# Kernel optimization log

Hardware: AMD Instinct MI355X
Metric: run time of the kernel (lower is better)

The kernel has to match this reference:

```python
import jax, jax.numpy as jnp
import numpy as np

N, E, IN_CH, HID, EDGE_DIM, L, G = 50000, 800000, 64, 128, 16, 3, 256

def _bn(h, g, b):
    # BatchNorm1d in training mode (biased batch variance), eps=1e-5
    m = h.mean(0)
    v = ((h - m) ** 2).mean(0)
    return (h - m) * jax.lax.rsqrt(v + 1e-5) * g + b

def setup_inputs() -> dict:
    key = jax.random.key(0)
    ks = jax.random.split(key, 24)
    s = 0.05
    inp = {
        'x': jax.random.normal(ks[0], (N, IN_CH), jnp.float32),
        'edge_attr': jax.random.uniform(ks[1], (E, EDGE_DIM), jnp.float32),
        'src': jax.random.randint(ks[2], (E,), 0, N, jnp.int32),
        'dst': jax.random.randint(ks[3], (E,), 0, N, jnp.int32),
        'batch': jnp.sort(jax.random.randint(ks[4], (N,), 0, G, jnp.int32)),
        'Wp': jax.random.normal(ks[5], (IN_CH, HID), jnp.float32) * s,
        'bp': jnp.zeros((HID,), jnp.float32),
        'conv_We': jax.random.normal(ks[6], (L, EDGE_DIM, HID), jnp.float32) * s,
        'conv_be': jnp.zeros((L, HID), jnp.float32),
        'conv_W1': jax.random.normal(ks[7], (L, HID, HID), jnp.float32) * s,
        'conv_b1': jnp.zeros((L, HID), jnp.float32),
        'conv_g1': jnp.ones((L, HID), jnp.float32),
        'conv_bt1': jnp.zeros((L, HID), jnp.float32),
        'conv_W2': jax.random.normal(ks[8], (L, HID, HID), jnp.float32) * s,
        'conv_b2': jnp.zeros((L, HID), jnp.float32),
        'bn_g': jnp.ones((L, HID), jnp.float32),
        'bn_b': jnp.zeros((L, HID), jnp.float32),
        'head_W1': jax.random.normal(ks[9], (HID * L * 2, HID), jnp.float32) * s,
        'head_b1': jnp.zeros((HID,), jnp.float32),
        'head_g': jnp.ones((HID,), jnp.float32),
        'head_bt': jnp.zeros((HID,), jnp.float32),
        'head_W2': jax.random.normal(ks[10], (HID, 1), jnp.float32) * s,
        'head_b2': jnp.zeros((1,), jnp.float32),
    }
    return inp

def reference(x, edge_attr, src, dst, batch, Wp, bp, conv_We, conv_be, conv_W1, conv_b1,
              conv_g1, conv_bt1, conv_W2, conv_b2, bn_g, bn_b, head_W1, head_b1,
              head_g, head_bt, head_W2, head_b2):
    n = x.shape[0]
    h = x @ Wp + bp  # [N, HID]
    outs = []
    for l in range(L):
        # GINEConv: msg = ReLU(x_src + lin(edge_attr)); sum-aggregate to dst; (1+eps)*x + agg, eps=0
        ee = edge_attr @ conv_We[l] + conv_be[l]          # [E, HID]
        msg = jax.nn.relu(h[src] + ee)                     # [E, HID]
        agg = jax.ops.segment_sum(msg, dst, num_segments=n)
        t = h + agg
        t = t @ conv_W1[l] + conv_b1[l]
        t = jax.nn.relu(_bn(t, conv_g1[l], conv_bt1[l]))
        t = t @ conv_W2[l] + conv_b2[l]
        h = jax.nn.relu(_bn(t, bn_g[l], bn_b[l]))          # outer BN + ReLU (dropout = identity, eval)
        outs.append(h)
    xj = jnp.concatenate(outs, axis=-1)                    # JK 'cat' -> [N, 3*HID]
    cnt = jax.ops.segment_sum(jnp.ones((n,), xj.dtype), batch, num_segments=G)
    z_mean = jax.ops.segment_sum(xj, batch, num_segments=G) / jnp.clip(cnt, 1.0)[:, None]
    z_max = jax.ops.segment_max(xj, batch, num_segments=G)
    z = jnp.concatenate([z_mean, z_max], axis=-1)          # [G, 6*HID]
    z = z @ head_W1 + head_b1
    z = jax.nn.relu(_bn(z, head_g, head_bt))
    return (z @ head_W2 + head_b2).squeeze(-1)             # [G]
```

## Files before the change

kernel.cpp:

```cpp
#include <hip/hip_runtime.h>
#include <hip/hip_bf16.h>
#include <hip/hip_fp16.h>

#define HID 128
#define EDIM 16

typedef float v4f __attribute__((ext_vector_type(4)));
typedef float v2f __attribute__((ext_vector_type(2)));
typedef short s8v __attribute__((ext_vector_type(8)));
typedef float f4v __attribute__((ext_vector_type(4)));
typedef unsigned int u8x __attribute__((ext_vector_type(8)));
typedef _Float16 h2v __attribute__((ext_vector_type(2)));

#define MFMA_BF16(a, b, c) __builtin_amdgcn_mfma_f32_16x16x32_bf16((a), (b), (c), 0, 0, 0)

__device__ __forceinline__ unsigned short bf16_rne(float v)
{
    unsigned u = __builtin_bit_cast(unsigned, v);
    return (unsigned short)((u + 0x7fffu + ((u >> 16) & 1u)) >> 16);
}

__device__ __forceinline__ unsigned pack2(float lo, float hi)
{
    return (unsigned)bf16_rne(lo) | ((unsigned)bf16_rne(hi) << 16);
}

__device__ __forceinline__ float bflo(unsigned u) { return __builtin_bit_cast(float, u << 16); }
__device__ __forceinline__ float bfhi(unsigned u) { return __builtin_bit_cast(float, u & 0xffff0000u); }

__device__ __forceinline__ v2f unpack2(unsigned u)
{
    v2f r; r.x = bflo(u); r.y = bfhi(u); return r;
}

__device__ __forceinline__ void split_bf16(float v, unsigned short& h, unsigned short& l)
{
    unsigned u = __builtin_bit_cast(unsigned, v);
    unsigned hu = (u + 0x7fffu + ((u >> 16) & 1u)) >> 16;
    h = (unsigned short)hu;
    float hf = __builtin_bit_cast(float, hu << 16);
    l = bf16_rne(v - hf);
}

__device__ __forceinline__ v2f vmax0(v2f a)
{
    v2f r; r.x = fmaxf(a.x, 0.f); r.y = fmaxf(a.y, 0.f); return r;
}

__device__ __forceinline__ unsigned pkh2(float lo, float hi)
{
    return (unsigned)__half_as_ushort(__float2half(lo)) |
           ((unsigned)__half_as_ushort(__float2half(hi)) << 16);
}

__device__ __forceinline__ void dot2(float& d, unsigned ea, unsigned w)
{
    d = __builtin_amdgcn_fdot2(__builtin_bit_cast(h2v, ea),
                               __builtin_bit_cast(h2v, w), d, false);
}

__global__ void hist_kernel(const int* __restrict__ dst, int* __restrict__ deg, int E)
{
    int e = blockIdx.x * 256 + threadIdx.x;
    if (e < E) atomicAdd(&deg[dst[e]], 1);
}

__global__ void block_sum_kernel(const int* __restrict__ deg, int* __restrict__ bsum, int Nn)
{
    int i = blockIdx.x * 256 + threadIdx.x;
    int v = (i < Nn) ? deg[i] : 0;
#pragma unroll
    for (int off = 32; off > 0; off >>= 1) v += __shfl_down(v, off, 64);
    __shared__ int ws[4];
    if ((threadIdx.x & 63) == 0) ws[threadIdx.x >> 6] = v;
    __syncthreads();
    if (threadIdx.x == 0) bsum[blockIdx.x] = ws[0] + ws[1] + ws[2] + ws[3];
}

__global__ void bsum_scan_kernel(int* bsum, int nb, int* total_out)
{
    __shared__ int sh[256];
    int tid = threadIdx.x;
    int v = (tid < nb) ? bsum[tid] : 0;
    sh[tid] = v;
    __syncthreads();
    for (int off = 1; off < 256; off <<= 1) {
        int tv = (tid >= off) ? sh[tid - off] : 0;
        __syncthreads();
        sh[tid] += tv;
        __syncthreads();
    }
    if (tid < nb) bsum[tid] = sh[tid] - v;
    if (tid == 255) *total_out = sh[255];
}

__global__ void block_scan_kernel(const int* __restrict__ deg, const int* __restrict__ bsum,
                                  int* __restrict__ row_start, int* __restrict__ cursor, int Nn)
{
    __shared__ int sh[256];
    int tid = threadIdx.x;
    int i = blockIdx.x * 256 + tid;
    int v = (i < Nn) ? deg[i] : 0;
    sh[tid] = v;
    __syncthreads();
    for (int off = 1; off < 256; off <<= 1) {
        int tv = (tid >= off) ? sh[tid - off] : 0;
        __syncthreads();
        sh[tid] += tv;
        __syncthreads();
    }
    if (i < Nn) {
        int excl = sh[tid] - v + bsum[blockIdx.x];
        row_start[i] = excl;
        cursor[i] = excl;
    }
}

__global__ void scatter_kernel(const int* __restrict__ src, const int* __restrict__ dst,
                               int* cursor, int* __restrict__ perm,
                               int* __restrict__ src_perm, int E)
{
    int e = blockIdx.x * 256 + threadIdx.x;
    if (e >= E) return;
    int pos = atomicAdd(&cursor[dst[e]], 1);
    perm[pos] = e;
    src_perm[pos] = src[e];
}

__global__ void gather_ea_f16(const float* __restrict__ ea, const int* __restrict__ perm,
                              unsigned* __restrict__ eaH, int E)
{
    int idx = blockIdx.x * 256 + threadIdx.x;
    int p = idx >> 1, hf = idx & 1;
    if (p >= E) return;
    int e = perm[p];
    const float* ap = &ea[(size_t)e * EDIM + hf * 8];
    float4 f0 = *(const float4*)ap;
    float4 f1 = *(const float4*)(ap + 4);
    uint4 o;
    o.x = pkh2(f0.x, f0.y);
    o.y = pkh2(f0.z, f0.w);
    o.z = pkh2(f1.x, f1.y);
    o.w = pkh2(f1.z, f1.w);
    *(uint4*)&eaH[(size_t)p * 8 + hf * 4] = o;
}

__global__ void prep_weights(const float* __restrict__ Wp, const float* __restrict__ W1,
                             const float* __restrict__ W2, unsigned short* __restrict__ out)
{
    int idx = blockIdx.x * 256 + threadIdx.x;
    if (idx < 8192) {
        int n = idx >> 6, k = idx & 63;
        unsigned short h, l;
        split_bf16(Wp[k * 128 + n], h, l);
        out[idx] = h;
        out[8192 + idx] = l;
    } else {
        int j = idx - 8192;
        if (j >= 6 * 16384) return;
        int m2 = j >> 14;
        int r = j & 16383;
        int n = r >> 7, k = r & 127;
        int l = m2 >> 1;
        const float* Wsrc = (m2 & 1) ? (W2 + l * 16384) : (W1 + l * 16384);
        unsigned short h, lo;
        split_bf16(Wsrc[k * 128 + n], h, lo);
        int base = 16384 + m2 * 32768;
        out[base + r] = h;
        out[base + 16384 + r] = lo;
    }
}

__device__ __forceinline__ void edge_f16(v2f& acc, v2f bj, unsigned hu, const u8x& e,
                                         const unsigned* __restrict__ wpk0,
                                         const unsigned* __restrict__ wpk1)
{
    float m0 = bj.x + bflo(hu);
    float m1 = bj.y + bfhi(hu);
#pragma unroll
    for (int kp = 0; kp < 8; ++kp) {
        dot2(m0, e[kp], wpk0[kp]);
        dot2(m1, e[kp], wpk1[kp]);
    }
    acc.x += fmaxf(m0, 0.f);
    acc.y += fmaxf(m1, 0.f);
}

__global__ __launch_bounds__(256, 8) void aggregate_f16(
    const unsigned short* __restrict__ h16, const unsigned* __restrict__ eaH,
    const int* __restrict__ src_perm, const int* __restrict__ row_start,
    const float* __restrict__ We, const float* __restrict__ be,
    float* __restrict__ t, int Nn)
{
    int tid = threadIdx.x;
    int lane = tid & 63;
    int c = lane * 2;
    unsigned wpk0[8], wpk1[8];
#pragma unroll
    for (int kp = 0; kp < 8; ++kp) {
        wpk0[kp] = pkh2(We[(2 * kp) * HID + c],     We[(2 * kp + 1) * HID + c]);
        wpk1[kp] = pkh2(We[(2 * kp) * HID + c + 1], We[(2 * kp + 1) * HID + c + 1]);
    }
    v2f bj = *(const v2f*)&be[c];
    int node = blockIdx.x * 4 + (tid >> 6);
    if (node >= Nn) return;
    const unsigned* __restrict__ hw = (const unsigned*)h16 + lane;
    v2f acc = unpack2(hw[(unsigned)node << 6]);
    int p0 = __builtin_amdgcn_readfirstlane(row_start[node]);
    int p1 = __builtin_amdgcn_readfirstlane(row_start[node + 1]);
    int p = p0;

    int s0 = 0, s1 = 0, s2 = 0, s3 = 0, s4 = 0, s5 = 0, s6 = 0, s7 = 0;
    unsigned hu0 = 0, hu1 = 0, hu2 = 0, hu3 = 0, hu4 = 0, hu5 = 0, hu6 = 0, hu7 = 0;
    if (p + 8 <= p1) {
        s0 = src_perm[p];     s1 = src_perm[p + 1]; s2 = src_perm[p + 2]; s3 = src_perm[p + 3];
        s4 = src_perm[p + 4]; s5 = src_perm[p + 5]; s6 = src_perm[p + 6]; s7 = src_perm[p + 7];
        hu0 = hw[(unsigned)s0 << 6]; hu1 = hw[(unsigned)s1 << 6];
        hu2 = hw[(unsigned)s2 << 6]; hu3 = hw[(unsigned)s3 << 6];
        hu4 = hw[(unsigned)s4 << 6]; hu5 = hw[(unsigned)s5 << 6];
        hu6 = hw[(unsigned)s6 << 6]; hu7 = hw[(unsigned)s7 << 6];
    }
    while (p + 8 <= p1) {
        int np = p + 8;
        u8x e0 = *(const u8x*)(eaH + (size_t)(unsigned)(p    ) * 8);
        u8x e1 = *(const u8x*)(eaH + (size_t)(unsigned)(p + 1) * 8);
        u8x e2 = *(const u8x*)(eaH + (size_t)(unsigned)(p + 2) * 8);
        u8x e3 = *(const u8x*)(eaH + (size_t)(unsigned)(p + 3) * 8);
        u8x e4 = *(const u8x*)(eaH + (size_t)(unsigned)(p + 4) * 8);
        u8x e5 = *(const u8x*)(eaH + (size_t)(unsigned)(p + 5) * 8);
        u8x e6 = *(const u8x*)(eaH + (size_t)(unsigned)(p + 6) * 8);
        u8x e7 = *(const u8x*)(eaH + (size_t)(unsigned)(p + 7) * 8);
        int t0 = 0, t1 = 0, t2 = 0, t3 = 0, t4 = 0, t5 = 0, t6 = 0, t7 = 0;
        unsigned hn0 = 0, hn1 = 0, hn2 = 0, hn3 = 0, hn4 = 0, hn5 = 0, hn6 = 0, hn7 = 0;
        if (np + 8 <= p1) {
            t0 = src_perm[np];     t1 = src_perm[np + 1]; t2 = src_perm[np + 2]; t3 = src_perm[np + 3];
            t4 = src_perm[np + 4]; t5 = src_perm[np + 5]; t6 = src_perm[np + 6]; t7 = src_perm[np + 7];
            hn0 = hw[(unsigned)t0 << 6]; hn1 = hw[(unsigned)t1 << 6];
            hn2 = hw[(unsigned)t2 << 6]; hn3 = hw[(unsigned)t3 << 6];
            hn4 = hw[(unsigned)t4 << 6]; hn5 = hw[(unsigned)t5 << 6];
            hn6 = hw[(unsigned)t6 << 6]; hn7 = hw[(unsigned)t7 << 6];
        }
        edge_f16(acc, bj, hu0, e0, wpk0, wpk1);
        edge_f16(acc, bj, hu1, e1, wpk0, wpk1);
        edge_f16(acc, bj, hu2, e2, wpk0, wpk1);
        edge_f16(acc, bj, hu3, e3, wpk0, wpk1);
        edge_f16(acc, bj, hu4, e4, wpk0, wpk1);
        edge_f16(acc, bj, hu5, e5, wpk0, wpk1);
        edge_f16(acc, bj, hu6, e6, wpk0, wpk1);
        edge_f16(acc, bj, hu7, e7, wpk0, wpk1);
        p = np;
        s0 = t0; s1 = t1; s2 = t2; s3 = t3; s4 = t4; s5 = t5; s6 = t6; s7 = t7;
        hu0 = hn0; hu1 = hn1; hu2 = hn2; hu3 = hn3;
        hu4 = hn4; hu5 = hn5; hu6 = hn6; hu7 = hn7;
    }
    for (; p < p1; ++p) {
        int s = src_perm[p];
        unsigned hu = hw[(unsigned)s << 6];
        u8x e = *(const u8x*)(eaH + (size_t)(unsigned)p * 8);
        edge_f16(acc, bj, hu, e, wpk0, wpk1);
    }
    *(v2f*)(t + ((unsigned)node << 7) + c) = acc;
}

__device__ __forceinline__ void matvp(const v4f& a0, const v4f& a1,
                                      const v4f& a2, const v4f& a3,
                                      const v2f* __restrict__ w, v2f& m)
{
    m += w[0] * a0.x;  m += w[1] * a0.y;  m += w[2] * a0.z;  m += w[3] * a0.w;
    m += w[4] * a1.x;  m += w[5] * a1.y;  m += w[6] * a1.z;  m += w[7] * a1.w;
    m += w[8] * a2.x;  m += w[9] * a2.y;  m += w[10] * a2.z; m += w[11] * a2.w;
    m += w[12] * a3.x; m += w[13] * a3.y; m += w[14] * a3.z; m += w[15] * a3.w;
}

__global__ __launch_bounds__(256, 8) void aggregate_fp32(
    const unsigned short* __restrict__ h16, const float* __restrict__ eaG,
    const int* __restrict__ perm, const int* __restrict__ src_perm,
    const int* __restrict__ row_start,
    const float* __restrict__ We, const float* __restrict__ be,
    float* __restrict__ t, int Nn)
{
    int tid = threadIdx.x;
    int lane = tid & 63;
    int c = lane * 2;
    v2f w[16];
#pragma unroll
    for (int k = 0; k < 16; ++k) w[k] = *(const v2f*)&We[k * HID + c];
    v2f bj = *(const v2f*)&be[c];
    int node = blockIdx.x * 4 + (tid >> 6);
    if (node >= Nn) return;
    const unsigned* __restrict__ hw = (const unsigned*)h16 + lane;
    v2f acc = unpack2(hw[(unsigned)node << 6]);
    int p0 = __builtin_amdgcn_readfirstlane(row_start[node]);
    int p1 = __builtin_amdgcn_readfirstlane(row_start[node + 1]);
    int p = p0;
    int s0 = 0, s1 = 0, s2 = 0, s3 = 0;
    if (p + 4 <= p1) { s0 = src_perm[p]; s1 = src_perm[p + 1]; s2 = src_perm[p + 2]; s3 = src_perm[p + 3]; }
    while (p + 4 <= p1) {
        int np = p + 4;
        int t0 = 0, t1 = 0, t2 = 0, t3 = 0;
        if (np + 4 <= p1) { t0 = src_perm[np]; t1 = src_perm[np + 1]; t2 = src_perm[np + 2]; t3 = src_perm[np + 3]; }
        unsigned hu0 = hw[(unsigned)s0 << 6];
        unsigned hu1 = hw[(unsigned)s1 << 6];
        unsigned hu2 = hw[(unsigned)s2 << 6];
        unsigned hu3 = hw[(unsigned)s3 << 6];
        int q0 = perm[p], q1 = perm[p + 1], q2 = perm[p + 2], q3 = perm[p + 3];
        const v4f* e0 = (const v4f*)(eaG + (size_t)(unsigned)q0 * EDIM);
        const v4f* e1 = (const v4f*)(eaG + (size_t)(unsigned)q1 * EDIM);
        const v4f* e2 = (const v4f*)(eaG + (size_t)(unsigned)q2 * EDIM);
        const v4f* e3 = (const v4f*)(eaG + (size_t)(unsigned)q3 * EDIM);
        v4f a00 = e0[0], a01 = e0[1], a02 = e0[2], a03 = e0[3];
        v4f a10 = e1[0], a11 = e1[1], a12 = e1[2], a13 = e1[3];
        v4f a20 = e2[0], a21 = e2[1], a22 = e2[2], a23 = e2[3];
        v4f a30 = e3[0], a31 = e3[1], a32 = e3[2], a33 = e3[3];
        v2f m0 = bj + unpack2(hu0), m1 = bj + unpack2(hu1);
        v2f m2 = bj + unpack2(hu2), m3 = bj + unpack2(hu3);
        matvp(a00, a01, a02, a03, w, m0);
        matvp(a10, a11, a12, a13, w, m1);
        matvp(a20, a21, a22, a23, w, m2);
        matvp(a30, a31, a32, a33, w, m3);
        acc += (vmax0(m0) + vmax0(m1)) + (vmax0(m2) + vmax0(m3));
        p = np;
        s0 = t0; s1 = t1; s2 = t2; s3 = t3;
    }
    for (; p < p1; ++p) {
        int s = src_perm[p];
        int q = perm[p];
        const v4f* e0 = (const v4f*)(eaG + (size_t)(unsigned)q * EDIM);
        v4f a0 = e0[0], a1 = e0[1], a2 = e0[2], a3 = e0[3];
        v2f m0 = bj + unpack2(hw[(unsigned)s << 6]);
        matvp(a0, a1, a2, a3, w, m0);
        acc += vmax0(m0);
    }
    *(v2f*)(t + ((unsigned)node << 7) + c) = acc;
}

#define LPAD 40

template<int K, bool PRE_BN, bool POST_STATS, bool OUT_BF16>
__global__ __launch_bounds__(256) void gemm_mfma(
    const float* __restrict__ A, const unsigned short* __restrict__ Wh,
    const unsigned short* __restrict__ Wl, const float* __restrict__ bias,
    const float* __restrict__ preStats, const float* __restrict__ preG, const float* __restrict__ preB,
    void* __restrict__ Cout, float* __restrict__ postStats, int Nrows, float invN)
{
    __shared__ __align__(16) unsigned short Ah[128 * LPAD], Al[128 * LPAD];
    __shared__ __align__(16) unsigned short Bh[128 * LPAD], Bl[128 * LPAD];
    __shared__ float sc[PRE_BN ? K : 1], sb[PRE_BN ? K : 1];
    int tid = threadIdx.x;
    int rbase = blockIdx.x * 128;
    if (PRE_BN) {
        if (tid < K) {
            float mean = preStats[tid] * invN;
            float var = preStats[K + tid] * invN - mean * mean;
            float rstd = rsqrtf(var + 1e-5f);
            float g = preG[tid];
            sc[tid] = rstd * g;
            sb[tid] = preB[tid] - mean * rstd * g;
        }
        __syncthreads();
    }
    int w = tid >> 6, nl = tid & 15, q = (tid >> 4) & 3;
    f4v acc[2][8];
#pragma unroll
    for (int mt = 0; mt < 2; ++mt)
#pragma unroll
        for (int nt = 0; nt < 8; ++nt)
#pragma unroll
            for (int r = 0; r < 4; ++r) acc[mt][nt][r] = 0.f;

    for (int ks = 0; ks < K / 32; ++ks) {
        int k0 = ks * 32;
        if (ks) __syncthreads();
#pragma unroll
        for (int i = 0; i < 4; ++i) {
            int cidx = tid + i * 256;
            int m = cidx >> 3, k4 = (cidx & 7) * 4;
            int gr = rbase + m;
            float4 v = make_float4(0.f, 0.f, 0.f, 0.f);
            if (gr < Nrows) v = *(const float4*)&A[(size_t)gr * K + k0 + k4];
            if (PRE_BN) {
                v.x = fmaxf(v.x * sc[k0 + k4]     + sb[k0 + k4],     0.f);
                v.y = fmaxf(v.y * sc[k0 + k4 + 1] + sb[k0 + k4 + 1], 0.f);
                v.z = fmaxf(v.z * sc[k0 + k4 + 2] + sb[k0 + k4 + 2], 0.f);
                v.w = fmaxf(v.w * sc[k0 + k4 + 3] + sb[k0 + k4 + 3], 0.f);
            }
            unsigned short h0, l0, h1, l1, h2, l2, h3, l3;
            split_bf16(v.x, h0, l0); split_bf16(v.y, h1, l1);
            split_bf16(v.z, h2, l2); split_bf16(v.w, h3, l3);
            uint2 hp, lp;
            hp.x = (unsigned)h0 | ((unsigned)h1 << 16); hp.y = (unsigned)h2 | ((unsigned)h3 << 16);
            lp.x = (unsigned)l0 | ((unsigned)l1 << 16); lp.y = (unsigned)l2 | ((unsigned)l3 << 16);
            *(uint2*)&Ah[m * LPAD + k4] = hp;
            *(uint2*)&Al[m * LPAD + k4] = lp;
        }
#pragma unroll
        for (int i = 0; i < 2; ++i) {
            int g = tid + i * 256;
            int n = g >> 2, kq = (g & 3) * 8;
            uint4 hv = *(const uint4*)&Wh[(size_t)n * K + k0 + kq];
            uint4 lv = *(const uint4*)&Wl[(size_t)n * K + k0 + kq];
            *(uint4*)&Bh[n * LPAD + kq] = hv;
            *(uint4*)&Bl[n * LPAD + kq] = lv;
        }
        __syncthreads();
        s8v ah0 = *(const s8v*)&Ah[(w * 32 + nl) * LPAD + q * 8];
        s8v ah1 = *(const s8v*)&Ah[(w * 32 + 16 + nl) * LPAD + q * 8];
        s8v al0 = *(const s8v*)&Al[(w * 32 + nl) * LPAD + q * 8];
        s8v al1 = *(const s8v*)&Al[(w * 32 + 16 + nl) * LPAD + q * 8];
#pragma unroll
        for (int nt = 0; nt < 8; ++nt) {
            s8v bh = *(const s8v*)&Bh[(nt * 16 + nl) * LPAD + q * 8];
            s8v bl = *(const s8v*)&Bl[(nt * 16 + nl) * LPAD + q * 8];
            acc[0][nt] = MFMA_BF16(ah0, bh, acc[0][nt]);
            acc[0][nt] = MFMA_BF16(ah0, bl, acc[0][nt]);
            acc[0][nt] = MFMA_BF16(al0, bh, acc[0][nt]);
            acc[1][nt] = MFMA_BF16(ah1, bh, acc[1][nt]);
            acc[1][nt] = MFMA_BF16(ah1, bl, acc[1][nt]);
            acc[1][nt] = MFMA_BF16(al1, bh, acc[1][nt]);
        }
    }
    __syncthreads();

    float* Cf = (float*)Cout;
    unsigned short* Ch = (unsigned short*)Cout;
    float* redS = (float*)Ah;
    float* redQ = (float*)Al;
#pragma unroll
    for (int nt = 0; nt < 8; ++nt) {
        int col = nt * 16 + nl;
        float bcol = bias[col];
        float sv = 0.f, qv = 0.f;
#pragma unroll
        for (int mt = 0; mt < 2; ++mt) {
#pragma unroll
            for (int r = 0; r < 4; ++r) {
                int grow = rbase + w * 32 + mt * 16 + q * 4 + r;
                if (grow < Nrows) {
                    float o = acc[mt][nt][r] + bcol;
                    if (OUT_BF16) Ch[(size_t)grow * HID + col] = bf16_rne(o);
                    else          Cf[(size_t)grow * HID + col] = o;
                    if (POST_STATS) { sv += o; qv += o * o; }
                }
            }
        }
        if (POST_STATS) {
            sv += __shfl_down(sv, 32, 64); sv += __shfl_down(sv, 16, 64);
            qv += __shfl_down(qv, 32, 64); qv += __shfl_down(qv, 16, 64);
            if ((tid & 63) < 16) { redS[w * 128 + col] = sv; redQ[w * 128 + col] = qv; }
        }
    }
    if (POST_STATS) {
        __syncthreads();
        if (tid < 128) {
            float S = redS[tid] + redS[128 + tid] + redS[256 + tid] + redS[384 + tid];
            float Q = redQ[tid] + redQ[128 + tid] + redQ[256 + tid] + redQ[384 + tid];
            atomicAdd(&postStats[tid], S);
            atomicAdd(&postStats[128 + tid], Q);
        }
    }
}

__global__ void bn_apply_pool(const float* __restrict__ X, unsigned short* __restrict__ h16,
                              const float* __restrict__ stats, const float* __restrict__ g,
                              const float* __restrict__ b, const int* __restrict__ starts,
                              float* __restrict__ z, int l, float invN)
{
    int gph = blockIdx.x;
    int tid = threadIdx.x;
    int ch4 = (tid & 31) * 4, wk = tid >> 5;
    float sc[4], sh[4];
#pragma unroll
    for (int u = 0; u < 4; ++u) {
        int j = ch4 + u;
        float mean = stats[j] * invN;
        float var = stats[128 + j] * invN - mean * mean;
        float rstd = rsqrtf(var + 1e-5f);
        float gg = g[j];
        sc[u] = rstd * gg;
        sh[u] = b[j] - mean * rstd * gg;
    }
    int s = starts[gph], e = starts[gph + 1];
    float4 sum = make_float4(0.f, 0.f, 0.f, 0.f);
    float4 mx = make_float4(0.f, 0.f, 0.f, 0.f);
    unsigned* hv32 = (unsigned*)h16;
    for (int n = s + wk; n < e; n += 16) {
        float4 v = *(const float4*)&X[(size_t)n * HID + ch4];
        v.x = fmaxf(v.x * sc[0] + sh[0], 0.f);
        v.y = fmaxf(v.y * sc[1] + sh[1], 0.f);
        v.z = fmaxf(v.z * sc[2] + sh[2], 0.f);
        v.w = fmaxf(v.w * sc[3] + sh[3], 0.f);
        uint2 pk;
        pk.x = pack2(v.x, v.y);
        pk.y = pack2(v.z, v.w);
        *(uint2*)&hv32[(size_t)n * 64 + (ch4 >> 1)] = pk;
        sum.x += v.x; sum.y += v.y; sum.z += v.z; sum.w += v.w;
        mx.x = fmaxf(mx.x, v.x); mx.y = fmaxf(mx.y, v.y);
        mx.z = fmaxf(mx.z, v.z); mx.w = fmaxf(mx.w, v.w);
    }
    __shared__ float ls[16 * 128], lm[16 * 128];
    *(float4*)&ls[wk * 128 + ch4] = sum;
    *(float4*)&lm[wk * 128 + ch4] = mx;
    __syncthreads();
    if (tid < 128) {
        float S = 0.f, M = 0.f;
#pragma unroll
        for (int k = 0; k < 16; ++k) {
            S += ls[k * 128 + tid];
            M = fmaxf(M, lm[k * 128 + tid]);
        }
        float cnt = (float)(e - s);
        z[(size_t)gph * 768 + l * 128 + tid] = S / fmaxf(cnt, 1.f);
        z[(size_t)gph * 768 + 384 + l * 128 + tid] = M;
    }
}

__global__ void starts_kernel(const int* __restrict__ batch, int* __restrict__ starts,
                              int Nn, int Gn)
{
    int g = blockIdx.x * blockDim.x + threadIdx.x;
    if (g > Gn) return;
    int lo = 0, hi = Nn;
    while (lo < hi) { int mid = (lo + hi) >> 1; if (batch[mid] < g) lo = mid + 1; else hi = mid; }
    starts[g] = lo;
}

__global__ void head_gemm1(const float* __restrict__ z, const float* __restrict__ W,
                           const float* __restrict__ bias, float* __restrict__ zr,
                           float* __restrict__ msums)
{
    __shared__ __align__(16) float zl[768];
    int g = blockIdx.x, j = threadIdx.x;
    for (int i = j; i < 768; i += 128) zl[i] = z[(size_t)g * 768 + i];
    __syncthreads();
    float acc = bias[j];
    for (int k = 0; k < 768; k += 4) {
        float4 a4 = *(const float4*)&zl[k];
        acc += a4.x * W[k * 128 + j] + a4.y * W[(k + 1) * 128 + j]
             + a4.z * W[(k + 2) * 128 + j] + a4.w * W[(k + 3) * 128 + j];
    }
    zr[(size_t)g * 128 + j] = acc;
    atomicAdd(&msums[j], acc);
    atomicAdd(&msums[128 + j], acc * acc);
}

__global__ void head_final(const float* __restrict__ zr, const float* __restrict__ msums,
                           const float* __restrict__ hg, const float* __restrict__ hb,
                           const float* __restrict__ W2, const float* __restrict__ b2,
                           float* __restrict__ out, float invG)
{
    int g = blockIdx.x, j = threadIdx.x;
    float mean = msums[j] * invG;
    float var = msums[128 + j] * invG - mean * mean;
    float rstd = rsqrtf(var + 1e-5f);
    float v = zr[(size_t)g * 128 + j];
    v = (v - mean) * rstd * hg[j] + hb[j];
    v = fmaxf(v, 0.f);
    float p = v * W2[j];
#pragma unroll
    for (int off = 32; off > 0; off >>= 1) p += __shfl_down(p, off, 64);
    __shared__ float partial[2];
    if ((j & 63) == 0) partial[j >> 6] = p;
    __syncthreads();
    if (j == 0) out[g] = partial[0] + partial[1] + b2[0];
}

extern "C" void kernel_launch(void* const* d_in, const int* in_sizes, int n_in,
                              void* d_out, int out_size, void* d_ws, size_t ws_size,
                              hipStream_t stream)
{
    const float* x         = (const float*)d_in[0];
    const float* edge_attr = (const float*)d_in[1];
    const int*   src       = (const int*)d_in[2];
    const int*   dst       = (const int*)d_in[3];
    const int*   batch     = (const int*)d_in[4];
    const float* Wp        = (const float*)d_in[5];
    const float* bp        = (const float*)d_in[6];
    const float* conv_We   = (const float*)d_in[7];
    const float* conv_be   = (const float*)d_in[8];
    const float* conv_W1   = (const float*)d_in[9];
    const float* conv_b1   = (const float*)d_in[10];
    const float* conv_g1   = (const float*)d_in[11];
    const float* conv_bt1  = (const float*)d_in[12];
    const float* conv_W2   = (const float*)d_in[13];
    const float* conv_b2   = (const float*)d_in[14];
    const float* bn_g      = (const float*)d_in[15];
    const float* bn_b      = (const float*)d_in[16];
    const float* head_W1   = (const float*)d_in[17];
    const float* head_b1   = (const float*)d_in[18];
    const float* head_g    = (const float*)d_in[19];
    const float* head_bt   = (const float*)d_in[20];
    const float* head_W2   = (const float*)d_in[21];
    const float* head_b2   = (const float*)d_in[22];

    const int N = in_sizes[4];
    const int E = in_sizes[2];
    const int G = out_size;
    const int L = 3;

    float* t        = (float*)d_ws;
    unsigned short* h16 = (unsigned short*)(t + (size_t)N * HID);
    float* z        = (float*)(h16 + (size_t)N * HID);
    float* zr       = z + (size_t)G * 768;
    float* statsAll = zr + (size_t)G * HID;
    int*   deg      = (int*)(statsAll + 7 * 256);
    int*   starts   = deg + N;
    int*   row_start= starts + (G + 1);
    int*   cursor   = row_start + (N + 1);
    int*   bsum     = cursor + N;
    int*   src_perm = bsum + 256;
    int*   perm     = src_perm + E;
    unsigned short* wt = (unsigned short*)(perm + E);
    size_t base_end = (size_t)((char*)(wt + 212992) - (char*)d_ws);
    size_t ea_off = (base_end + 63) & ~(size_t)63;
    bool gath = (ea_off + (size_t)E * 8 * sizeof(unsigned)) <= ws_size;
    unsigned* eaH = (unsigned*)((char*)d_ws + ea_off);
    float* msums = statsAll + 6 * 256;

    (void)n_in;

    const float invN = 1.0f / (float)N;
    const float invG = 1.0f / (float)G;
    const int nb = (N + 255) / 256;
    const int gemmBlocks = (N + 127) / 128;

    (void)hipMemsetAsync(statsAll, 0, 7 * 256 * sizeof(float) + (size_t)N * sizeof(int), stream);
    hist_kernel<<<(E + 255) / 256, 256, 0, stream>>>(dst, deg, E);
    block_sum_kernel<<<nb, 256, 0, stream>>>(deg, bsum, N);
    bsum_scan_kernel<<<1, 256, 0, stream>>>(bsum, nb, &row_start[N]);
    block_scan_kernel<<<nb, 256, 0, stream>>>(deg, bsum, row_start, cursor, N);
    scatter_kernel<<<(E + 255) / 256, 256, 0, stream>>>(src, dst, cursor, perm, src_perm, E);
    if (gath)
        gather_ea_f16<<<(E * 2 + 255) / 256, 256, 0, stream>>>(edge_attr, perm, eaH, E);
    starts_kernel<<<1, 512, 0, stream>>>(batch, starts, N, G);
    prep_weights<<<(8192 + 6 * 16384 + 255) / 256, 256, 0, stream>>>(Wp, conv_W1, conv_W2, wt);

    const unsigned short* Wp_hi = wt;
    const unsigned short* Wp_lo = wt + 8192;

    gemm_mfma<64, false, false, true><<<gemmBlocks, 256, 0, stream>>>(
        x, Wp_hi, Wp_lo, bp, nullptr, nullptr, nullptr, h16, nullptr, N, invN);

    for (int l = 0; l < L; ++l) {
        float* sI = statsAll + l * 512;
        float* sO = sI + 256;
        const unsigned short* W1hi = wt + 16384 + (size_t)(2 * l) * 32768;
        const unsigned short* W1lo = W1hi + 16384;
        const unsigned short* W2hi = wt + 16384 + (size_t)(2 * l + 1) * 32768;
        const unsigned short* W2lo = W2hi + 16384;
        if (gath)
            aggregate_f16<<<(N + 3) / 4, 256, 0, stream>>>(
                h16, eaH, src_perm, row_start,
                conv_We + (size_t)l * EDIM * HID, conv_be + l * HID, t, N);
        else
            aggregate_fp32<<<(N + 3) / 4, 256, 0, stream>>>(
                h16, edge_attr, perm, src_perm, row_start,
                conv_We + (size_t)l * EDIM * HID, conv_be + l * HID, t, N);
        gemm_mfma<128, false, true, false><<<gemmBlocks, 256, 0, stream>>>(
            t, W1hi, W1lo, conv_b1 + l * HID,
            nullptr, nullptr, nullptr, t, sI, N, invN);
        gemm_mfma<128, true, true, false><<<gemmBlocks, 256, 0, stream>>>(
            t, W2hi, W2lo, conv_b2 + l * HID,
            sI, conv_g1 + l * HID, conv_bt1 + l * HID, t, sO, N, invN);
        bn_apply_pool<<<G, 512, 0, stream>>>(
            t, h16, sO, bn_g + l * HID, bn_b + l * HID, starts, z, l, invN);
    }

    head_gemm1<<<G, 128, 0, stream>>>(z, head_W1, head_b1, zr, msums);
    head_final<<<G, 128, 0, stream>>>(zr, msums, head_g, head_bt, head_W2, head_b2,
                                      (float*)d_out, invG);
}
```

Measured before the change: 669.2 us.

## Restructure edge aggregation into a 2-edge software pipeline with prepacked f16 weights

Edge weights are now prepacked into f16 pairs once per layer by a new prep kernel, replacing per-thread packing inside the aggregation kernel. The aggregation loop moves from 8-edge unrolled batches with a scalar tail to a 2-edge-per-iteration pipeline. Source indices are prefetched two steps ahead, and edge-attribute and h loads one step ahead, with clamped indices so there is no tail loop. A VGPR-zero offset forces edge-attr and src loads down the vector path, and the occupancy hint drops from 8 to 6 waves. Less memory-level parallelism per wave is traded for lower register pressure and no tail handling.

Result: slower. 750.1 us (+12.1%).

```diff
diff --git a/kernel.cpp b/kernel.cpp
--- a/kernel.cpp
+++ b/kernel.cpp
@@ -9,7 +9,6 @@
 typedef float v2f __attribute__((ext_vector_type(2)));
 typedef short s8v __attribute__((ext_vector_type(8)));
 typedef float f4v __attribute__((ext_vector_type(4)));
-typedef unsigned int u8x __attribute__((ext_vector_type(8)));
 typedef _Float16 h2v __attribute__((ext_vector_type(2)));
 
 #define MFMA_BF16(a, b, c) __builtin_amdgcn_mfma_f32_16x16x32_bf16((a), (b), (c), 0, 0, 0)
@@ -171,93 +170,101 @@
     }
 }
 
-__device__ __forceinline__ void edge_f16(v2f& acc, v2f bj, unsigned hu, const u8x& e,
-                                         const unsigned* __restrict__ wpk0,
-                                         const unsigned* __restrict__ wpk1)
+__global__ void prep_wef16(const float* __restrict__ We, unsigned* __restrict__ out)
+{
+    int idx = blockIdx.x * 256 + threadIdx.x;
+    if (idx >= 3 * 1024) return;
+    int l = idx >> 10, r = idx & 1023, ch = r >> 3, kp = r & 7;
+    const float* W = We + (size_t)l * EDIM * HID;
+    out[idx] = pkh2(W[(2 * kp) * HID + ch], W[(2 * kp + 1) * HID + ch]);
+}
+
+__device__ __forceinline__ void edgeD(v2f& acc, v2f bj, unsigned hu,
+                                      uint4 ea, uint4 eb,
+                                      uint4 w0a, uint4 w0b, uint4 w1a, uint4 w1b)
 {
     float m0 = bj.x + bflo(hu);
     float m1 = bj.y + bfhi(hu);
-#pragma unroll
-    for (int kp = 0; kp < 8; ++kp) {
-        dot2(m0, e[kp], wpk0[kp]);
-        dot2(m1, e[kp], wpk1[kp]);
-    }
+    dot2(m0, ea.x, w0a.x); dot2(m1, ea.x, w1a.x);
+    dot2(m0, ea.y, w0a.y); dot2(m1, ea.y, w1a.y);
+    dot2(m0, ea.z, w0a.z); dot2(m1, ea.z, w1a.z);
+    dot2(m0, ea.w, w0a.w); dot2(m1, ea.w, w1a.w);
+    dot2(m0, eb.x, w0b.x); dot2(m1, eb.x, w1b.x);
+    dot2(m0, eb.y, w0b.y); dot2(m1, eb.y, w1b.y);
+    dot2(m0, eb.z, w0b.z); dot2(m1, eb.z, w1b.z);
+    dot2(m0, eb.w, w0b.w); dot2(m1, eb.w, w1b.w);
     acc.x += fmaxf(m0, 0.f);
     acc.y += fmaxf(m1, 0.f);
 }
 
-__global__ __launch_bounds__(256, 8) void aggregate_f16(
+__global__ __launch_bounds__(256, 6) void aggregate_f16(
     const unsigned short* __restrict__ h16, const unsigned* __restrict__ eaH,
     const int* __restrict__ src_perm, const int* __restrict__ row_start,
-    const float* __restrict__ We, const float* __restrict__ be,
+    const unsigned* __restrict__ Wpk, const float* __restrict__ be,
     float* __restrict__ t, int Nn)
 {
     int tid = threadIdx.x;
     int lane = tid & 63;
     int c = lane * 2;
-    unsigned wpk0[8], wpk1[8];
-#pragma unroll
-    for (int kp = 0; kp < 8; ++kp) {
-        wpk0[kp] = pkh2(We[(2 * kp) * HID + c],     We[(2 * kp + 1) * HID + c]);
-        wpk1[kp] = pkh2(We[(2 * kp) * HID + c + 1], We[(2 * kp + 1) * HID + c + 1]);
-    }
-    v2f bj = *(const v2f*)&be[c];
     int node = blockIdx.x * 4 + (tid >> 6);
     if (node >= Nn) return;
+    const uint4* wrow = (const uint4*)(Wpk + (size_t)c * 8);
+    uint4 w0a = wrow[0], w0b = wrow[1];
+    uint4 w1a = wrow[2], w1b = wrow[3];
+    v2f bj = *(const v2f*)&be[c];
+    unsigned zz;
+    asm("v_mov_b32 %0, 0" : "=v"(zz));
+    const unsigned* __restrict__ eaV = eaH + zz;
+    const int* __restrict__ spV = src_perm + zz;
     const unsigned* __restrict__ hw = (const unsigned*)h16 + lane;
     v2f acc = unpack2(hw[(unsigned)node << 6]);
     int p0 = __builtin_amdgcn_readfirstlane(row_start[node]);
     int p1 = __builtin_amdgcn_readfirstlane(row_start[node + 1]);
     int p = p0;
 
-    int s0 = 0, s1 = 0, s2 = 0, s3 = 0, s4 = 0, s5 = 0, s6 = 0, s7 = 0;
-    unsigned hu0 = 0, hu1 = 0, hu2 = 0, hu3 = 0, hu4 = 0, hu5 = 0, hu6 = 0, hu7 = 0;
-    if (p + 8 <= p1) {
-        s0 = src_perm[p];     s1 = src_perm[p + 1]; s2 = src_perm[p + 2]; s3 = src_perm[p + 3];
-        s4 = src_perm[p + 4]; s5 = src_perm[p + 5]; s6 = src_perm[p + 6]; s7 = src_perm[p + 7];
-        hu0 = hw[(unsigned)s0 << 6]; hu1 = hw[(unsigned)s1 << 6];
-        hu2 = hw[(unsigned)s2 << 6]; hu3 = hw[(unsigned)s3 << 6];
-        hu4 = hw[(unsigned)s4 << 6]; hu5 = hw[(unsigned)s5 << 6];
-        hu6 = hw[(unsigned)s6 << 6]; hu7 = hw[(unsigned)s7 << 6];
-    }
-    while (p + 8 <= p1) {
-        int np = p + 8;
-        u8x e0 = *(const u8x*)(eaH + (size_t)(unsigned)(p    ) * 8);
-        u8x e1 = *(const u8x*)(eaH + (size_t)(unsigned)(p + 1) * 8);
-        u8x e2 = *(const u8x*)(eaH + (size_t)(unsigned)(p + 2) * 8);
-        u8x e3 = *(const u8x*)(eaH + (size_t)(unsigned)(p + 3) * 8);
-        u8x e4 = *(const u8x*)(eaH + (size_t)(unsigned)(p + 4) * 8);
-        u8x e5 = *(const u8x*)(eaH + (size_t)(unsigned)(p + 5) * 8);
-        u8x e6 = *(const u8x*)(eaH + (size_t)(unsigned)(p + 6) * 8);
-        u8x e7 = *(const u8x*)(eaH + (size_t)(unsigned)(p + 7) * 8);
-        int t0 = 0, t1 = 0, t2 = 0, t3 = 0, t4 = 0, t5 = 0, t6 = 0, t7 = 0;
-        unsigned hn0 = 0, hn1 = 0, hn2 = 0, hn3 = 0, hn4 = 0, hn5 = 0, hn6 = 0, hn7 = 0;
-        if (np + 8 <= p1) {
-            t0 = src_perm[np];     t1 = src_perm[np + 1]; t2 = src_perm[np + 2]; t3 = src_perm[np + 3];
-            t4 = src_perm[np + 4]; t5 = src_perm[np + 5]; t6 = src_perm[np + 6]; t7 = src_perm[np + 7];
-            hn0 = hw[(unsigned)t0 << 6]; hn1 = hw[(unsigned)t1 << 6];
-            hn2 = hw[(unsigned)t2 << 6]; hn3 = hw[(unsigned)t3 << 6];
-            hn4 = hw[(unsigned)t4 << 6]; hn5 = hw[(unsigned)t5 << 6];
-            hn6 = hw[(unsigned)t6 << 6]; hn7 = hw[(unsigned)t7 << 6];
-        }
-        edge_f16(acc, bj, hu0, e0, wpk0, wpk1);
-        edge_f16(acc, bj, hu1, e1, wpk0, wpk1);
-        edge_f16(acc, bj, hu2, e2, wpk0, wpk1);
-        edge_f16(acc, bj, hu3, e3, wpk0, wpk1);
-        edge_f16(acc, bj, hu4, e4, wpk0, wpk1);
-        edge_f16(acc, bj, hu5, e5, wpk0, wpk1);
-        edge_f16(acc, bj, hu6, e6, wpk0, wpk1);
-        edge_f16(acc, bj, hu7, e7, wpk0, wpk1);
+    int s10 = 0, s11 = 0;
+    unsigned hu0 = 0, hu1 = 0;
+    uint4 e0 = {0, 0, 0, 0}, e1 = {0, 0, 0, 0};
+    uint4 e2 = {0, 0, 0, 0}, e3 = {0, 0, 0, 0};
+    if (p < p1) {
+        int q0 = p;
+        int q1 = (p + 1 < p1) ? p + 1 : p;
+        int q2 = (p + 2 < p1) ? p + 2 : q1;
+        int q3 = (p + 3 < p1) ? p + 3 : q2;
+        int sc0 = spV[q0], sc1 = spV[q1];
+        s10 = spV[q2]; s11 = spV[q3];
+        hu0 = hw[(unsigned)sc0 << 6];
+        hu1 = hw[(unsigned)sc1 << 6];
+        e0 = *(const uint4*)(eaV + (size_t)(unsigned)q0 * 8);
+        e1 = *(const uint4*)(eaV + (size_t)(unsigned)q0 * 8 + 4);
+        e2 = *(const uint4*)(eaV + (size_t)(unsigned)q1 * 8);
+        e3 = *(const uint4*)(eaV + (size_t)(unsigned)q1 * 8 + 4);
+    }
+    while (p < p1) {
+        int np = p + 2;
+        int s20 = 0, s21 = 0;
+        unsigned hn0 = 0, hn1 = 0;
+        uint4 n0 = e0, n1 = e1, n2 = e2, n3 = e3;
+        if (np < p1) {
+            int qa = np;
+            int qb = (np + 1 < p1) ? np + 1 : np;
+            int qc = (np + 2 < p1) ? np + 2 : qb;
+            int qd = (np + 3 < p1) ? np + 3 : qc;
+            s20 = spV[qc]; s21 = spV[qd];
+            hn0 = hw[(unsigned)s10 << 6];
+            hn1 = hw[(unsigned)s11 << 6];
+            n0 = *(const uint4*)(eaV + (size_t)(unsigned)qa * 8);
+            n1 = *(const uint4*)(eaV + (size_t)(unsigned)qa * 8 + 4);
+            n2 = *(const uint4*)(eaV + (size_t)(unsigned)qb * 8);
+            n3 = *(const uint4*)(eaV + (size_t)(unsigned)qb * 8 + 4);
+        }
+        edgeD(acc, bj, hu0, e0, e1, w0a, w0b, w1a, w1b);
+        if (p + 1 < p1)
+            edgeD(acc, bj, hu1, e2, e3, w0a, w0b, w1a, w1b);
         p = np;
-        s0 = t0; s1 = t1; s2 = t2; s3 = t3; s4 = t4; s5 = t5; s6 = t6; s7 = t7;
-        hu0 = hn0; hu1 = hn1; hu2 = hn2; hu3 = hn3;
-        hu4 = hn4; hu5 = hn5; hu6 = hn6; hu7 = hn7;
-    }
-    for (; p < p1; ++p) {
-        int s = src_perm[p];
-        unsigned hu = hw[(unsigned)s << 6];
-        u8x e = *(const u8x*)(eaH + (size_t)(unsigned)p * 8);
-        edge_f16(acc, bj, hu, e, wpk0, wpk1);
+        hu0 = hn0; hu1 = hn1;
+        e0 = n0; e1 = n1; e2 = n2; e3 = n3;
+        s10 = s20; s11 = s21;
     }
     *(v2f*)(t + ((unsigned)node << 7) + c) = acc;
 }
@@ -610,7 +617,8 @@
     int*   src_perm = bsum + 256;
     int*   perm     = src_perm + E;
     unsigned short* wt = (unsigned short*)(perm + E);
-    size_t base_end = (size_t)((char*)(wt + 212992) - (char*)d_ws);
+    unsigned* wef   = (unsigned*)(wt + 212992);
+    size_t base_end = (size_t)((char*)(wef + 3 * 1024) - (char*)d_ws);
     size_t ea_off = (base_end + 63) & ~(size_t)63;
     bool gath = (ea_off + (size_t)E * 8 * sizeof(unsigned)) <= ws_size;
     unsigned* eaH = (unsigned*)((char*)d_ws + ea_off);
@@ -633,6 +641,7 @@
         gather_ea_f16<<<(E * 2 + 255) / 256, 256, 0, stream>>>(edge_attr, perm, eaH, E);
     starts_kernel<<<1, 512, 0, stream>>>(batch, starts, N, G);
     prep_weights<<<(8192 + 6 * 16384 + 255) / 256, 256, 0, stream>>>(Wp, conv_W1, conv_W2, wt);
+    prep_wef16<<<(3 * 1024 + 255) / 256, 256, 0, stream>>>(conv_We, wef);
 
     const unsigned short* Wp_hi = wt;
     const unsigned short* Wp_lo = wt + 8192;
@@ -649,8 +658,8 @@
         const unsigned short* W2lo = W2hi + 16384;
         if (gath)
             aggregate_f16<<<(N + 3) / 4, 256, 0, stream>>>(
-                h16, eaH, src_perm, row_start,
-                conv_We + (size_t)l * EDIM * HID, conv_be + l * HID, t, N);
+                h16, eaH, src_perm, row_start, wef + (size_t)l * 1024,
+                conv_be + l * HID, t, N);
         else
             aggregate_fp32<<<(N + 3) / 4, 256, 0, stream>>>(
                 h16, edge_attr, perm, src_perm, row_start,
```
